# Performance work log

Hardware: AMD Instinct MI355X
Metric: run time of the kernel (lower is better)

Reference implementation:

```python
import jax, jax.numpy as jnp
import numpy as np

VOCAB, EMB, HID = 32000, 256, 512
B, S = 4, 512


def setup_inputs() -> dict:
    key = jax.random.key(0)
    ks = jax.random.split(key, 8)
    sc_e = 1.0  # torch nn.Embedding default: N(0,1)
    k_lstm = 1.0 / np.sqrt(HID)
    k_lin = 1.0 / np.sqrt(HID)
    emb = jax.random.normal(ks[0], (VOCAB, EMB), dtype=jnp.float32) * sc_e
    emb = emb.at[0].set(0.0)  # padding_idx=0 row is zero
    w_ih = jax.random.uniform(ks[1], (4 * HID, EMB), minval=-k_lstm, maxval=k_lstm)
    w_hh = jax.random.uniform(ks[2], (4 * HID, HID), minval=-k_lstm, maxval=k_lstm)
    b_ih = jax.random.uniform(ks[3], (4 * HID,), minval=-k_lstm, maxval=k_lstm)
    b_hh = jax.random.uniform(ks[4], (4 * HID,), minval=-k_lstm, maxval=k_lstm)
    W = jax.random.uniform(ks[5], (VOCAB, HID), minval=-k_lin, maxval=k_lin)
    b = jax.random.uniform(ks[6], (VOCAB,), minval=-k_lin, maxval=k_lin)
    batch = jax.random.randint(ks[7], (B, S), 0, VOCAB, dtype=jnp.int64 if jax.config.jax_enable_x64 else jnp.int32)
    return {"batch": batch, "emb": emb, "w_ih": w_ih, "w_hh": w_hh,
            "b_ih": b_ih, "b_hh": b_hh, "W": W, "b": b}


def _lstm(x, w_ih, w_hh, b_ih, b_hh):
    # x: [B, S, E]; torch gate order i, f, g, o; h0 = c0 = 0
    H = w_hh.shape[1]
    bsz = x.shape[0]
    xp = jnp.einsum('bse,ge->bsg', x, w_ih) + b_ih + b_hh  # [B,S,4H]
    xp = jnp.swapaxes(xp, 0, 1)  # [S,B,4H]

    def step(carry, xt):
        h, c = carry
        g = xt + h @ w_hh.T
        i, f, gg, o = jnp.split(g, 4, axis=-1)
        i, f, o = jax.nn.sigmoid(i), jax.nn.sigmoid(f), jax.nn.sigmoid(o)
        c = f * c + i * jnp.tanh(gg)
        h = o * jnp.tanh(c)
        return (h, c), h

    h0 = jnp.zeros((bsz, H), x.dtype)
    _, hs = jax.lax.scan(step, (h0, h0), xp)
    return jnp.swapaxes(hs, 0, 1)  # [B,S,H]


def reference(batch, emb, w_ih, w_hh, b_ih, b_hh, W, b):
    embeds = emb[batch]                               # [B,S,E]
    lstm_out = _lstm(embeds, w_ih, w_hh, b_ih, b_hh)  # [B,S,H]
    logits = jnp.einsum('bsh,vh->bsv', lstm_out, W) + b
    scores = jax.nn.log_softmax(logits, axis=2)       # [B,S,V]
    # Faithful to torch: contiguous view (row-major reinterpretation)
    V = W.shape[0]
    bsz = batch.shape[0]
    scores2 = scores.reshape(-1, V, bsz)              # [S,V,B]
    tgt2 = batch.reshape(-1, bsz)                     # [S,B]
    picked = jnp.take_along_axis(scores2, tgt2[:, None, :], axis=1)[:, 0, :]
    return -jnp.mean(picked)
```

## Files before the change

### kernel.cpp

```cpp
#include <hip/hip_runtime.h>
#include <hip/hip_bf16.h>
#include <math.h>

#define VOCAB 32000
#define EMB   256
#define HID   512
#define BB    4
#define SS    512
#define G4H   2048
#define BS    2048

typedef unsigned int   u32;
typedef unsigned short u16;
using short8 = __attribute__((ext_vector_type(8))) short;
using f32x4  = __attribute__((ext_vector_type(4))) float;

#define OFF_HSB  8192000ull
#define OFF_HW   8716288ull
#define OFF_FLG  8720384ull
#define OFF_SUM  8722432ull

__device__ inline unsigned packbf(float a, float b) {
    unsigned ua = __float_as_uint(a), ub = __float_as_uint(b);
    ua += 0x7fffu + ((ua >> 16) & 1u);
    ub += 0x7fffu + ((ub >> 16) & 1u);
    return (ua >> 16) | (ub & 0xffff0000u);
}

#define GLOAD_LDS16(gp, lp) __builtin_amdgcn_global_load_lds( \
    (const __attribute__((address_space(1))) void*)(gp),      \
    (__attribute__((address_space(3))) void*)(lp), 16, 0, 0)

__global__ __launch_bounds__(256) void k_embed_xp(
    const int* __restrict__ batch, const float* __restrict__ emb,
    const float* __restrict__ w_ih, const float* __restrict__ b_ih,
    const float* __restrict__ b_hh, float* __restrict__ xp)
{
    __shared__ float Asl[16 * 64];
    __shared__ float Bsl[16 * 64];
    const int tid = threadIdx.x;
    const int bs0 = blockIdx.x * 64;
    const int g0  = blockIdx.y * 64;
    const int m  = tid & 63;
    const int kg = tid >> 6;
    const int tok = batch[bs0 + m];
    const float* arow = emb + (size_t)tok * EMB;
    const float* brow = w_ih + (size_t)(g0 + m) * EMB;
    const int tm = tid >> 4;
    const int tv = tid & 15;

    float acc[4][4] = {};
    for (int k0 = 0; k0 < EMB; k0 += 16) {
        float4 a4 = *(const float4*)(arow + k0 + kg * 4);
        float4 b4 = *(const float4*)(brow + k0 + kg * 4);
        __syncthreads();
        const int kb = kg * 4;
        Asl[(kb + 0) * 64 + m] = a4.x;
        Asl[(kb + 1) * 64 + m] = a4.y;
        Asl[(kb + 2) * 64 + m] = a4.z;
        Asl[(kb + 3) * 64 + m] = a4.w;
        Bsl[(kb + 0) * 64 + m] = b4.x;
        Bsl[(kb + 1) * 64 + m] = b4.y;
        Bsl[(kb + 2) * 64 + m] = b4.z;
        Bsl[(kb + 3) * 64 + m] = b4.w;
        __syncthreads();
#pragma unroll
        for (int k = 0; k < 16; ++k) {
            float4 av = *(const float4*)&Asl[k * 64 + tm * 4];
            float4 bv = *(const float4*)&Bsl[k * 64 + tv * 4];
            float a[4] = {av.x, av.y, av.z, av.w};
            float bb[4] = {bv.x, bv.y, bv.z, bv.w};
#pragma unroll
            for (int i = 0; i < 4; ++i)
#pragma unroll
                for (int j = 0; j < 4; ++j)
                    acc[i][j] += a[i] * bb[j];
        }
    }
    float bsum[4];
#pragma unroll
    for (int j = 0; j < 4; ++j) {
        int g = g0 + tv * 4 + j;
        bsum[j] = b_ih[g] + b_hh[g];
    }
#pragma unroll
    for (int i = 0; i < 4; ++i) {
        int row = bs0 + tm * 4 + i;
        float4 o;
        o.x = acc[i][0] + bsum[0];
        o.y = acc[i][1] + bsum[1];
        o.z = acc[i][2] + bsum[2];
        o.w = acc[i][3] + bsum[3];
        *(float4*)(xp + (size_t)row * G4H + g0 + tv * 4) = o;
    }
}

__global__ __launch_bounds__(512) void k_lstm(
    const float* __restrict__ w_hh, const float* __restrict__ xp,
    u32* __restrict__ hw, u16* __restrict__ hsaveB)
{
    __shared__ float hl[4 * 132];
    __shared__ float gacc[128];
    __shared__ float xs[128];

    const int tid   = threadIdx.x;
    const int wg    = blockIdx.x;
    const int c     = wg >> 4;
    const int slice = wg & 15;
    const int j0    = slice * 32;
    const int r     = tid >> 2;
    const int q     = tid & 3;
    const int grow  = (r >> 5) * HID + j0 + (r & 31);

    unsigned wreg[64];
    {
        const float* wsrc = w_hh + (size_t)grow * HID + q * 128;
#pragma unroll
        for (int i = 0; i < 32; ++i) {
            float4 f = *(const float4*)(wsrc + i * 4);
            wreg[2 * i]     = packbf(f.x, f.y);
            wreg[2 * i + 1] = packbf(f.z, f.w);
        }
    }

    float cst = 0.f;

    for (int t = 0; t < SS; ++t) {
        const int p = t & 1;
        if (tid < 128)
            xs[tid] = xp[(size_t)(c * SS + t) * G4H +
                         (tid >> 5) * HID + j0 + (tid & 31)];
        {
            u32* addr = hw + p * (BB * HID) + c * HID + tid;
            u32 w;
            int guard = 0;
            for (;;) {
                w = __hip_atomic_load(addr, __ATOMIC_RELAXED,
                                      __HIP_MEMORY_SCOPE_AGENT);
                if ((w & 0xffffu) == (u32)t) break;
                __builtin_amdgcn_s_sleep(1);
                if (++guard > 2000000) break;
            }
            hl[(tid >> 7) * 132 + (tid & 127)] = __uint_as_float(w & 0xffff0000u);
        }
        __syncthreads();

        float acc = 0.f;
        {
            const float2* hq = (const float2*)(hl + q * 132);
#pragma unroll
            for (int kp = 0; kp < 64; ++kp) {
                unsigned w2 = wreg[kp];
                float2 h2 = hq[kp];
                acc = fmaf(h2.x, __uint_as_float(w2 << 16), acc);
                acc = fmaf(h2.y, __uint_as_float(w2 & 0xffff0000u), acc);
            }
        }
        acc += __shfl_xor(acc, 1);
        acc += __shfl_xor(acc, 2);
        if (q == 0) gacc[r] = acc + xs[r];
        __syncthreads();

        if (tid < 32) {
            float iv = gacc[tid],      fv = gacc[32 + tid];
            float gv = gacc[64 + tid], ov = gacc[96 + tid];
            float si = 1.f / (1.f + __expf(-iv));
            float sf = 1.f / (1.f + __expf(-fv));
            float so = 1.f / (1.f + __expf(-ov));
            cst = sf * cst + si * tanhf(gv);
            float hv = so * tanhf(cst);
            unsigned u = __float_as_uint(hv);
            u += 0x7fffu + ((u >> 16) & 1u);
            u &= 0xffff0000u;
            __hip_atomic_store(hw + (p ^ 1) * (BB * HID) + c * HID + j0 + tid,
                               u | (u32)(t + 1), __ATOMIC_RELAXED,
                               __HIP_MEMORY_SCOPE_AGENT);
            hsaveB[(size_t)(c * SS + t) * HID + j0 + tid] = (u16)(u >> 16);
        }
    }
}

__global__ __launch_bounds__(256) void k_wcvt(
    const float* __restrict__ W, u16* __restrict__ WB)
{
    int i = blockIdx.x * 256 + threadIdx.x;
    float4 f = ((const float4*)W)[i];
    uint2 o;
    o.x = packbf(f.x, f.y);
    o.y = packbf(f.z, f.w);
    ((uint2*)WB)[i] = o;
}

__global__ __launch_bounds__(256) void k_logits_lse(
    const u16* __restrict__ hsaveB, const u16* __restrict__ WB,
    const float* __restrict__ bias, float* __restrict__ sumexp)
{
    __shared__ u16 As[128 * 64];
    __shared__ u16 Bs[128 * 64];
    const int tid  = threadIdx.x;
    const int lane = tid & 63;
    const int wave = tid >> 6;
    const int wr   = wave >> 1;
    const int wc   = wave & 1;
    const int bs0  = blockIdx.x * 128;
    const int v0   = blockIdx.y * 128;
    const int lr   = lane & 15;
    const int lc   = lane >> 4;

    f32x4 acc[4][4];
#pragma unroll
    for (int m = 0; m < 4; ++m)
#pragma unroll
        for (int n = 0; n < 4; ++n)
            acc[m][n] = (f32x4){0.f, 0.f, 0.f, 0.f};

    for (int k0 = 0; k0 < HID; k0 += 64) {
#pragma unroll
        for (int it = 0; it < 4; ++it) {
            int base = it * 256 + wave * 64;
            int idx  = base + lane;
            int row  = idx >> 3, cl = idx & 7;
            int gcl  = cl ^ (row & 7);
            const u16* gA = hsaveB + (size_t)(bs0 + row) * HID + k0 + gcl * 8;
            GLOAD_LDS16(gA, As + (size_t)base * 8);
            const u16* gB = WB + (size_t)(v0 + row) * HID + k0 + gcl * 8;
            GLOAD_LDS16(gB, Bs + (size_t)base * 8);
        }
        asm volatile("s_waitcnt vmcnt(0)" ::: "memory");
        __syncthreads();

        short8 af[4][2], bf[4][2];
#pragma unroll
        for (int m = 0; m < 4; ++m)
#pragma unroll
            for (int ks = 0; ks < 2; ++ks) {
                int rowA = wr * 64 + m * 16 + lr;
                int swa  = ((ks * 4 + lc) ^ (rowA & 7)) * 8;
                af[m][ks] = *(const short8*)&As[rowA * 64 + swa];
                int rowB = wc * 64 + m * 16 + lr;
                int swb  = ((ks * 4 + lc) ^ (rowB & 7)) * 8;
                bf[m][ks] = *(const short8*)&Bs[rowB * 64 + swb];
            }
#pragma unroll
        for (int m = 0; m < 4; ++m)
#pragma unroll
            for (int n = 0; n < 4; ++n)
#pragma unroll
                for (int ks = 0; ks < 2; ++ks)
                    acc[m][n] = __builtin_amdgcn_mfma_f32_16x16x32_bf16(
                        af[m][ks], bf[n][ks], acc[m][n], 0, 0, 0);
        __syncthreads();
    }

    float bn[4];
#pragma unroll
    for (int n = 0; n < 4; ++n)
        bn[n] = bias[v0 + wc * 64 + n * 16 + lr];

#pragma unroll
    for (int m = 0; m < 4; ++m) {
        float p0 = 0.f, p1 = 0.f, p2 = 0.f, p3 = 0.f;
#pragma unroll
        for (int n = 0; n < 4; ++n) {
            float b = bn[n];
            p0 += __expf(acc[m][n][0] + b);
            p1 += __expf(acc[m][n][1] + b);
            p2 += __expf(acc[m][n][2] + b);
            p3 += __expf(acc[m][n][3] + b);
        }
#pragma unroll
        for (int off = 1; off < 16; off <<= 1) {
            p0 += __shfl_xor(p0, off);
            p1 += __shfl_xor(p1, off);
            p2 += __shfl_xor(p2, off);
            p3 += __shfl_xor(p3, off);
        }
        if (lr == 0) {
            int row = bs0 + wr * 64 + m * 16 + lc * 4;
            atomicAdd(&sumexp[row + 0], p0);
            atomicAdd(&sumexp[row + 1], p1);
            atomicAdd(&sumexp[row + 2], p2);
            atomicAdd(&sumexp[row + 3], p3);
        }
    }
}

__device__ inline float dotp(u32 h, u32 w) {
    return __uint_as_float(h << 16) * __uint_as_float(w << 16) +
           __uint_as_float(h & 0xffff0000u) * __uint_as_float(w & 0xffff0000u);
}

__global__ __launch_bounds__(256) void k_final(
    const int* __restrict__ batch, const u16* __restrict__ hsaveB,
    const u16* __restrict__ WB, const float* __restrict__ bias,
    const float* __restrict__ sumexp, float* __restrict__ out)
{
    const int gt   = blockIdx.x * 256 + threadIdx.x;
    const int wid  = gt >> 6;
    const int lane = gt & 63;
    const unsigned tgt = (unsigned)batch[wid];
    const unsigned s2 = wid >> 2, b2 = wid & 3;
    const unsigned j = s2 * (VOCAB * BB) + tgt * BB + b2;
    const unsigned SV = (unsigned)SS * VOCAB;
    const unsigned b_o = j / SV;
    const unsigned rr = j - b_o * SV;
    const unsigned s_o = rr / VOCAB;
    const unsigned v_o = rr - s_o * VOCAB;
    const unsigned row = b_o * SS + s_o;

    uint4 hu = *(const uint4*)(hsaveB + (size_t)row * HID + lane * 8);
    uint4 wu = *(const uint4*)(WB + (size_t)v_o * HID + lane * 8);
    float d = dotp(hu.x, wu.x) + dotp(hu.y, wu.y) +
              dotp(hu.z, wu.z) + dotp(hu.w, wu.w);
#pragma unroll
    for (int off = 32; off >= 1; off >>= 1)
        d += __shfl_xor(d, off);
    if (lane == 0) {
        float picked = d + bias[v_o] - logf(sumexp[row]);
        atomicAdd(out, -picked * (1.f / (float)BS));
    }
}

extern "C" void kernel_launch(void* const* d_in, const int* in_sizes, int n_in,
                              void* d_out, int out_size, void* d_ws, size_t ws_size,
                              hipStream_t stream)
{
    const int*   batch = (const int*)d_in[0];
    const float* emb   = (const float*)d_in[1];
    const float* w_ih  = (const float*)d_in[2];
    const float* w_hh  = (const float*)d_in[3];
    const float* b_ih  = (const float*)d_in[4];
    const float* b_hh  = (const float*)d_in[5];
    const float* Wm    = (const float*)d_in[6];
    const float* bvec  = (const float*)d_in[7];
    float* out = (float*)d_out;
    float* ws  = (float*)d_ws;

    float* xp      = ws;
    u16*   WB      = (u16*)ws;
    u16*   hsaveB  = (u16*)(ws + OFF_HSB);
    u32*   hw      = (u32*)(ws + OFF_HW);
    float* sumexp  = ws + OFF_SUM;

    hipMemsetAsync(hw, 0, (4096 + 2048 + 2048) * sizeof(float), stream);
    hipMemsetAsync(out, 0, sizeof(float), stream);

    dim3 g1(BS / 64, G4H / 64);
    k_embed_xp<<<g1, 256, 0, stream>>>(batch, emb, w_ih, b_ih, b_hh, xp);

    k_lstm<<<64, 512, 0, stream>>>(w_hh, xp, hw, hsaveB);

    k_wcvt<<<VOCAB * HID / 4 / 256, 256, 0, stream>>>(Wm, WB);

    dim3 g3(BS / 128, VOCAB / 128);
    k_logits_lse<<<g3, 256, 0, stream>>>(hsaveB, WB, bvec, sumexp);

    k_final<<<BS * 64 / 256, 256, 0, stream>>>(batch, hsaveB, WB, bvec, sumexp, out);
}
```

Measured before the change: 1.142 ms.

## Spread LSTM recurrence over 128 workgroups with wave-local gate reduction

The persistent LSTM kernel now runs 128 workgroups, each owning 16 hidden units, so every thread keeps half as many bf16 weight registers and each dot product covers 64 elements instead of 128. All four gates of a unit are reduced in registers with cross-lane shuffles, so the second barrier and the shared-memory gate buffer go away. The h buffer in shared memory is double-buffered by parity, and tanh is computed from a single exp. The costs are more workgroups polling the global flags each step and slightly different tanh rounding.

```diff
diff --git a/kernel.cpp b/kernel.cpp
--- a/kernel.cpp
+++ b/kernel.cpp
@@ -17,7 +17,6 @@
 
 #define OFF_HSB  8192000ull
 #define OFF_HW   8716288ull
-#define OFF_FLG  8720384ull
 #define OFF_SUM  8722432ull
 
 __device__ inline unsigned packbf(float a, float b) {
@@ -25,6 +24,10 @@
     ua += 0x7fffu + ((ua >> 16) & 1u);
     ub += 0x7fffu + ((ub >> 16) & 1u);
     return (ua >> 16) | (ub & 0xffff0000u);
+}
+
+__device__ inline float fast_tanh(float x) {
+    return 1.f - 2.f / (__expf(2.f * x) + 1.f);
 }
 
 #define GLOAD_LDS16(gp, lp) __builtin_amdgcn_global_load_lds( \
@@ -99,24 +102,24 @@
     const float* __restrict__ w_hh, const float* __restrict__ xp,
     u32* __restrict__ hw, u16* __restrict__ hsaveB)
 {
-    __shared__ float hl[4 * 132];
-    __shared__ float gacc[128];
-    __shared__ float xs[128];
+    __shared__ float hl[2][8 * 68];
 
     const int tid   = threadIdx.x;
     const int wg    = blockIdx.x;
-    const int c     = wg >> 4;
-    const int slice = wg & 15;
-    const int j0    = slice * 32;
-    const int r     = tid >> 2;
-    const int q     = tid & 3;
-    const int grow  = (r >> 5) * HID + j0 + (r & 31);
-
-    unsigned wreg[64];
+    const int c     = wg >> 5;
+    const int slice = wg & 31;
+    const int j0    = slice * 16;
+    const int u     = tid >> 5;
+    const int g     = (tid >> 3) & 3;
+    const int q     = tid & 7;
+    const int lane  = tid & 63;
+    const int grow  = g * HID + j0 + u;
+
+    unsigned wreg[32];
     {
-        const float* wsrc = w_hh + (size_t)grow * HID + q * 128;
-#pragma unroll
-        for (int i = 0; i < 32; ++i) {
+        const float* wsrc = w_hh + (size_t)grow * HID + q * 64;
+#pragma unroll
+        for (int i = 0; i < 16; ++i) {
             float4 f = *(const float4*)(wsrc + i * 4);
             wreg[2 * i]     = packbf(f.x, f.y);
             wreg[2 * i + 1] = packbf(f.z, f.w);
@@ -127,12 +130,12 @@
 
     for (int t = 0; t < SS; ++t) {
         const int p = t & 1;
-        if (tid < 128)
-            xs[tid] = xp[(size_t)(c * SS + t) * G4H +
-                         (tid >> 5) * HID + j0 + (tid & 31)];
+        float xsv = 0.f;
+        if (q == 0)
+            xsv = xp[(size_t)(c * SS + t) * G4H + grow];
+        u32 w;
         {
             u32* addr = hw + p * (BB * HID) + c * HID + tid;
-            u32 w;
             int guard = 0;
             for (;;) {
                 w = __hip_atomic_load(addr, __ATOMIC_RELAXED,
@@ -141,41 +144,45 @@
                 __builtin_amdgcn_s_sleep(1);
                 if (++guard > 2000000) break;
             }
-            hl[(tid >> 7) * 132 + (tid & 127)] = __uint_as_float(w & 0xffff0000u);
-        }
+        }
+        hl[p][(tid >> 6) * 68 + (tid & 63)] = __uint_as_float(w & 0xffff0000u);
         __syncthreads();
 
         float acc = 0.f;
         {
-            const float2* hq = (const float2*)(hl + q * 132);
-#pragma unroll
-            for (int kp = 0; kp < 64; ++kp) {
-                unsigned w2 = wreg[kp];
-                float2 h2 = hq[kp];
-                acc = fmaf(h2.x, __uint_as_float(w2 << 16), acc);
-                acc = fmaf(h2.y, __uint_as_float(w2 & 0xffff0000u), acc);
+            const float4* h4 = (const float4*)&hl[p][q * 68];
+#pragma unroll
+            for (int k = 0; k < 16; ++k) {
+                float4 hv = h4[k];
+                unsigned wa = wreg[2 * k], wb = wreg[2 * k + 1];
+                acc = fmaf(hv.x, __uint_as_float(wa << 16), acc);
+                acc = fmaf(hv.y, __uint_as_float(wa & 0xffff0000u), acc);
+                acc = fmaf(hv.z, __uint_as_float(wb << 16), acc);
+                acc = fmaf(hv.w, __uint_as_float(wb & 0xffff0000u), acc);
             }
         }
         acc += __shfl_xor(acc, 1);
         acc += __shfl_xor(acc, 2);
-        if (q == 0) gacc[r] = acc + xs[r];
-        __syncthreads();
-
-        if (tid < 32) {
-            float iv = gacc[tid],      fv = gacc[32 + tid];
-            float gv = gacc[64 + tid], ov = gacc[96 + tid];
-            float si = 1.f / (1.f + __expf(-iv));
-            float sf = 1.f / (1.f + __expf(-fv));
-            float so = 1.f / (1.f + __expf(-ov));
-            cst = sf * cst + si * tanhf(gv);
-            float hv = so * tanhf(cst);
-            unsigned u = __float_as_uint(hv);
-            u += 0x7fffu + ((u >> 16) & 1u);
-            u &= 0xffff0000u;
-            __hip_atomic_store(hw + (p ^ 1) * (BB * HID) + c * HID + j0 + tid,
-                               u | (u32)(t + 1), __ATOMIC_RELAXED,
+        acc += __shfl_xor(acc, 4);
+        acc += xsv;
+        const int base = lane & 32;
+        float s_i = __shfl(acc, base + 0);
+        float s_f = __shfl(acc, base + 8);
+        float s_g = __shfl(acc, base + 16);
+        float s_o = __shfl(acc, base + 24);
+        if ((lane & 31) == 0) {
+            float si = 1.f / (1.f + __expf(-s_i));
+            float sf = 1.f / (1.f + __expf(-s_f));
+            float so = 1.f / (1.f + __expf(-s_o));
+            cst = sf * cst + si * fast_tanh(s_g);
+            float hv = so * fast_tanh(cst);
+            unsigned uu = __float_as_uint(hv);
+            uu += 0x7fffu + ((uu >> 16) & 1u);
+            uu &= 0xffff0000u;
+            __hip_atomic_store(hw + (p ^ 1) * (BB * HID) + c * HID + j0 + u,
+                               uu | (u32)(t + 1), __ATOMIC_RELAXED,
                                __HIP_MEMORY_SCOPE_AGENT);
-            hsaveB[(size_t)(c * SS + t) * HID + j0 + tid] = (u16)(u >> 16);
+            hsaveB[(size_t)(c * SS + t) * HID + j0 + u] = (u16)(uu >> 16);
         }
     }
 }
@@ -348,7 +355,7 @@
     dim3 g1(BS / 64, G4H / 64);
     k_embed_xp<<<g1, 256, 0, stream>>>(batch, emb, w_ih, b_ih, b_hh, xp);
 
-    k_lstm<<<64, 512, 0, stream>>>(w_hh, xp, hw, hsaveB);
+    k_lstm<<<128, 512, 0, stream>>>(w_hh, xp, hw, hsaveB);
 
     k_wcvt<<<VOCAB * HID / 4 / 256, 256, 0, stream>>>(Wm, WB);
 
```

After: 1.447 ms. +26.8%, slower.

## Re-layout xp per LSTM slice, split recurrent dot into four accumulators, fast tanh

Applied to the files above, without the earlier changes.

The input-projection kernel now writes xp in a [chain, slice, t, 128] layout, so each LSTM workgroup reads its 128 gate pre-activations contiguously. Every thread loads its own value straight into a register, which removes the shared-memory xs staging. The recurrent dot product uses float4 LDS reads and four independent accumulators to shorten the FMA dependency chain. tanhf is replaced by an exp-based fast tanh on the serial critical path, at some cost in accuracy.

```diff
diff --git a/kernel.cpp b/kernel.cpp
--- a/kernel.cpp
+++ b/kernel.cpp
@@ -17,7 +17,6 @@
 
 #define OFF_HSB  8192000ull
 #define OFF_HW   8716288ull
-#define OFF_FLG  8720384ull
 #define OFF_SUM  8722432ull
 
 __device__ inline unsigned packbf(float a, float b) {
@@ -25,6 +24,13 @@
     ua += 0x7fffu + ((ua >> 16) & 1u);
     ub += 0x7fffu + ((ub >> 16) & 1u);
     return (ua >> 16) | (ub & 0xffff0000u);
+}
+
+__device__ inline float lo16(unsigned w) { return __uint_as_float(w << 16); }
+__device__ inline float hi16(unsigned w) { return __uint_as_float(w & 0xffff0000u); }
+
+__device__ inline float fast_tanh(float x) {
+    return 1.f - 2.f / (__expf(2.f * x) + 1.f);
 }
 
 #define GLOAD_LDS16(gp, lp) __builtin_amdgcn_global_load_lds( \
@@ -83,25 +89,31 @@
         int g = g0 + tv * 4 + j;
         bsum[j] = b_ih[g] + b_hh[g];
     }
+    const int cg = g0 + tv * 4;
+    const int gg = cg >> 9;
+    const int jj = cg & 511;
+    const int sl = jj >> 5;
+    const int li = jj & 31;
 #pragma unroll
     for (int i = 0; i < 4; ++i) {
         int row = bs0 + tm * 4 + i;
+        int cch = row >> 9, tt = row & 511;
         float4 o;
         o.x = acc[i][0] + bsum[0];
         o.y = acc[i][1] + bsum[1];
         o.z = acc[i][2] + bsum[2];
         o.w = acc[i][3] + bsum[3];
-        *(float4*)(xp + (size_t)row * G4H + g0 + tv * 4) = o;
+        *(float4*)(xp + ((size_t)(cch * 16 + sl) * SS + tt) * 128 +
+                   gg * 32 + li) = o;
     }
 }
 
 __global__ __launch_bounds__(512) void k_lstm(
-    const float* __restrict__ w_hh, const float* __restrict__ xp,
+    const float* __restrict__ w_hh, const float* __restrict__ xp2,
     u32* __restrict__ hw, u16* __restrict__ hsaveB)
 {
     __shared__ float hl[4 * 132];
     __shared__ float gacc[128];
-    __shared__ float xs[128];
 
     const int tid   = threadIdx.x;
     const int wg    = blockIdx.x;
@@ -123,16 +135,15 @@
         }
     }
 
+    const float* xbase = xp2 + (size_t)(c * 16 + slice) * (SS * 128) + r;
     float cst = 0.f;
 
     for (int t = 0; t < SS; ++t) {
         const int p = t & 1;
-        if (tid < 128)
-            xs[tid] = xp[(size_t)(c * SS + t) * G4H +
-                         (tid >> 5) * HID + j0 + (tid & 31)];
+        float xsv = xbase[t * 128];
+        u32 w;
         {
             u32* addr = hw + p * (BB * HID) + c * HID + tid;
-            u32 w;
             int guard = 0;
             for (;;) {
                 w = __hip_atomic_load(addr, __ATOMIC_RELAXED,
@@ -141,24 +152,45 @@
                 __builtin_amdgcn_s_sleep(1);
                 if (++guard > 2000000) break;
             }
-            hl[(tid >> 7) * 132 + (tid & 127)] = __uint_as_float(w & 0xffff0000u);
-        }
-        __syncthreads();
-
-        float acc = 0.f;
+        }
+        hl[(tid >> 7) * 132 + (tid & 127)] = __uint_as_float(w & 0xffff0000u);
+        __syncthreads();
+
+        float a0 = 0.f, a1 = 0.f, a2 = 0.f, a3 = 0.f;
         {
-            const float2* hq = (const float2*)(hl + q * 132);
-#pragma unroll
-            for (int kp = 0; kp < 64; ++kp) {
-                unsigned w2 = wreg[kp];
-                float2 h2 = hq[kp];
-                acc = fmaf(h2.x, __uint_as_float(w2 << 16), acc);
-                acc = fmaf(h2.y, __uint_as_float(w2 & 0xffff0000u), acc);
+            const float4* h4 = (const float4*)&hl[q * 132];
+#pragma unroll
+            for (int k = 0; k < 32; k += 4) {
+                float4 v0 = h4[k + 0];
+                unsigned wa = wreg[2 * k + 0], wb = wreg[2 * k + 1];
+                a0 = fmaf(v0.x, lo16(wa), a0);
+                a0 = fmaf(v0.y, hi16(wa), a0);
+                a0 = fmaf(v0.z, lo16(wb), a0);
+                a0 = fmaf(v0.w, hi16(wb), a0);
+                float4 v1 = h4[k + 1];
+                wa = wreg[2 * k + 2]; wb = wreg[2 * k + 3];
+                a1 = fmaf(v1.x, lo16(wa), a1);
+                a1 = fmaf(v1.y, hi16(wa), a1);
+                a1 = fmaf(v1.z, lo16(wb), a1);
+                a1 = fmaf(v1.w, hi16(wb), a1);
+                float4 v2 = h4[k + 2];
+                wa = wreg[2 * k + 4]; wb = wreg[2 * k + 5];
+                a2 = fmaf(v2.x, lo16(wa), a2);
+                a2 = fmaf(v2.y, hi16(wa), a2);
+                a2 = fmaf(v2.z, lo16(wb), a2);
+                a2 = fmaf(v2.w, hi16(wb), a2);
+                float4 v3 = h4[k + 3];
+                wa = wreg[2 * k + 6]; wb = wreg[2 * k + 7];
+                a3 = fmaf(v3.x, lo16(wa), a3);
+                a3 = fmaf(v3.y, hi16(wa), a3);
+                a3 = fmaf(v3.z, lo16(wb), a3);
+                a3 = fmaf(v3.w, hi16(wb), a3);
             }
         }
+        float acc = (a0 + a1) + (a2 + a3);
         acc += __shfl_xor(acc, 1);
         acc += __shfl_xor(acc, 2);
-        if (q == 0) gacc[r] = acc + xs[r];
+        if (q == 0) gacc[r] = acc + xsv;
         __syncthreads();
 
         if (tid < 32) {
@@ -167,15 +199,15 @@
             float si = 1.f / (1.f + __expf(-iv));
             float sf = 1.f / (1.f + __expf(-fv));
             float so = 1.f / (1.f + __expf(-ov));
-            cst = sf * cst + si * tanhf(gv);
-            float hv = so * tanhf(cst);
-            unsigned u = __float_as_uint(hv);
-            u += 0x7fffu + ((u >> 16) & 1u);
-            u &= 0xffff0000u;
+            cst = sf * cst + si * fast_tanh(gv);
+            float hv = so * fast_tanh(cst);
+            unsigned uu = __float_as_uint(hv);
+            uu += 0x7fffu + ((uu >> 16) & 1u);
+            uu &= 0xffff0000u;
             __hip_atomic_store(hw + (p ^ 1) * (BB * HID) + c * HID + j0 + tid,
-                               u | (u32)(t + 1), __ATOMIC_RELAXED,
+                               uu | (u32)(t + 1), __ATOMIC_RELAXED,
                                __HIP_MEMORY_SCOPE_AGENT);
-            hsaveB[(size_t)(c * SS + t) * HID + j0 + tid] = (u16)(u >> 16);
+            hsaveB[(size_t)(c * SS + t) * HID + j0 + tid] = (u16)(uu >> 16);
         }
     }
 }
```

New measurement: 1.145 ms. Within noise of the previous version (+0.3%).
